# Optimization experiments

Hardware: AMD Instinct MI355X
Metric: run time of the kernel (lower is better)

## Reference

```python
import jax, jax.numpy as jnp
import numpy as np

DEPTH, DIM, DFF, VOCAB = 4, 512, 2048, 4096
EPS = 1e-5

def layernorm(x, w, b):
    mu = jnp.mean(x, axis=-1, keepdims=True)
    var = jnp.mean((x - mu) ** 2, axis=-1, keepdims=True)
    return (x - mu) * jax.lax.rsqrt(var + EPS) * w + b

def sconv(x, phazor_c, last_conv_c):
    # x: [B,L,dim] real; phazor_c, last_conv_c: [dim] complex
    B, L, D = x.shape
    r = jnp.abs(phazor_c)
    p = jnp.tanh(r) * jnp.exp(1j * jnp.angle(phazor_c))          # [dim]
    prog = p[None, :] ** jnp.arange(L, dtype=jnp.float32)[:, None]  # [L,dim]
    filt_fft = jnp.fft.fft(prog, n=2 * L, axis=0)                # [2L,dim]
    x_fft = jnp.fft.fft(x.astype(jnp.complex64), n=2 * L, axis=1)  # [B,2L,dim]
    conv = jnp.fft.ifft(filt_fft[None] * x_fft, axis=1)[:, :L]   # [B,L,dim]
    conv = conv + last_conv_c[None, None, :] * prog[None] * p[None, None, :]
    return conv.real.astype(x.dtype)

def setup_inputs() -> dict:
    key = jax.random.key(0)
    ks = jax.random.split(key, 20)
    f32 = jnp.float32
    inp = {}
    inp['x'] = jax.random.normal(ks[0], (2, 4096, VOCAB), dtype=f32)
    inp['Win'] = jax.random.normal(ks[1], (DIM, VOCAB), dtype=f32) * VOCAB ** -0.5
    inp['bin'] = jnp.zeros((DIM,), f32)
    inp['ln1_w'] = jnp.ones((DEPTH, DIM), f32)
    inp['ln1_b'] = jnp.zeros((DEPTH, DIM), f32)
    # phazor init: exp(2*pi*i*arange/dim)*|randn|
    ang = 2 * np.pi * jnp.arange(DIM, dtype=f32) / DIM
    mag = jnp.abs(jax.random.normal(ks[2], (DEPTH, DIM), dtype=f32))
    inp['phz_re'] = mag * jnp.cos(ang)[None]
    inp['phz_im'] = mag * jnp.sin(ang)[None]
    inp['lc_re'] = jax.random.normal(ks[3], (DEPTH, DIM), dtype=f32)
    inp['lc_im'] = jax.random.normal(ks[4], (DEPTH, DIM), dtype=f32)
    inp['sc_lin'] = jnp.ones((DEPTH, DIM), f32)
    inp['ln2_w'] = jnp.ones((DEPTH, DIM), f32)
    inp['ln2_b'] = jnp.zeros((DEPTH, DIM), f32)
    inp['W1'] = jax.random.normal(ks[5], (DEPTH, DFF, DIM), dtype=f32) * DIM ** -0.5
    inp['b1'] = jnp.zeros((DEPTH, DFF), f32)
    inp['W2'] = jax.random.normal(ks[6], (DEPTH, DIM, DFF), dtype=f32) * DFF ** -0.5
    inp['b2'] = jnp.zeros((DEPTH, DIM), f32)
    inp['lnl_w'] = jnp.ones((DIM,), f32)
    inp['lnl_b'] = jnp.zeros((DIM,), f32)
    inp['Wout'] = jax.random.normal(ks[7], (VOCAB, DIM), dtype=f32) * DIM ** -0.5
    inp['bout'] = jnp.zeros((VOCAB,), f32)
    return inp

def _forward(x, Win, bin, ln1_w, ln1_b, phz_re, phz_im, lc_re, lc_im, sc_lin,
             ln2_w, ln2_b, W1, b1, W2, b2, lnl_w, lnl_b, Wout, bout):
    h = jnp.einsum('blv,dv->bld', x, Win) + bin  # token_in

    def body(h, p):
        l1w, l1b, pr, pi, lr, li, scl, l2w, l2b, w1, b1_, w2, b2_ = p
        y = jax.nn.silu(layernorm(h, l1w, l1b))
        y = sconv(y, pr + 1j * pi, lr + 1j * li)
        h = h + y * scl
        y = layernorm(h, l2w, l2b)
        y = jax.nn.silu(jnp.einsum('bld,fd->blf', y, w1) + b1_)
        y = jnp.einsum('blf,df->bld', y, w2) + b2_
        return h + y, None

    xs = (ln1_w, ln1_b, phz_re, phz_im, lc_re, lc_im, sc_lin,
          ln2_w, ln2_b, W1, b1, W2, b2)
    h, _ = jax.lax.scan(body, h, xs)
    h = layernorm(h, lnl_w, lnl_b)
    return jnp.einsum('bld,vd->blv', h, Wout) + bout

def reference(x, Win, bin, ln1_w, ln1_b, phz_re, phz_im, lc_re, lc_im, sc_lin,
              ln2_w, ln2_b, W1, b1, W2, b2, lnl_w, lnl_b, Wout, bout):
    return _forward(x, Win, bin, ln1_w, ln1_b, phz_re, phz_im, lc_re, lc_im,
                    sc_lin, ln2_w, ln2_b, W1, b1, W2, b2, lnl_w, lnl_b, Wout, bout)
```

## Files before the change

### kernel.cpp

```cpp
#include <hip/hip_runtime.h>
#include <hip/hip_bf16.h>
#include <cstdint>
#include <cstddef>

#define DEPTH 4
#define DIM 512
#define DFF 2048
#define VOCAB 4096
#define NB 2
#define LSEQ 4096
#define MR (NB*LSEQ)
#define EPSL 1e-5f
#define NC 128
#define TCH 32

typedef __attribute__((ext_vector_type(8))) short  s8v;
typedef __attribute__((ext_vector_type(4))) float  f4v;
typedef __attribute__((ext_vector_type(8))) __bf16 bf8v;

__device__ __forceinline__ unsigned short f2b(float f) {
  union { float f; unsigned int u; } v; v.f = f;
  unsigned int r = v.u + 0x7FFFu + ((v.u >> 16) & 1u);
  return (unsigned short)(r >> 16);
}

__device__ __forceinline__ void gld16(const void* g, void* l) {
  __builtin_amdgcn_global_load_lds(
      (const __attribute__((address_space(1))) unsigned int*)(uintptr_t)g,
      (__attribute__((address_space(3))) unsigned int*)(uintptr_t)l,
      16, 0, 0);
}

__global__ void __launch_bounds__(256) cvt_f32_bf16(
    const float* __restrict__ in, unsigned short* __restrict__ out, int n8)
{
  int i = blockIdx.x * 256 + threadIdx.x;
  if (i >= n8) return;
  const f4v* p = (const f4v*)(in + (size_t)i * 8);
  f4v a = p[0], b = p[1];
  s8v o;
  o[0]=(short)f2b(a[0]); o[1]=(short)f2b(a[1]); o[2]=(short)f2b(a[2]); o[3]=(short)f2b(a[3]);
  o[4]=(short)f2b(b[0]); o[5]=(short)f2b(b[1]); o[6]=(short)f2b(b[2]); o[7]=(short)f2b(b[3]);
  *(s8v*)(out + (size_t)i * 8) = o;
}

template<int MODE>
__global__ void __launch_bounds__(256) ln_kernel(
    const float* __restrict__ x, const float* __restrict__ w, const float* __restrict__ b,
    float* __restrict__ outf, unsigned short* __restrict__ outb)
{
  int row  = blockIdx.x * 4 + (threadIdx.x >> 6);
  int lane = threadIdx.x & 63;
  const float* xp = x + (size_t)row * DIM + lane * 8;
  f4v v0 = *(const f4v*)xp;
  f4v v1 = *(const f4v*)(xp + 4);
  float s = 0.f, s2 = 0.f;
#pragma unroll
  for (int j = 0; j < 4; ++j) { s += v0[j]; s2 += v0[j]*v0[j]; s += v1[j]; s2 += v1[j]*v1[j]; }
#pragma unroll
  for (int off = 32; off; off >>= 1) { s += __shfl_xor(s, off, 64); s2 += __shfl_xor(s2, off, 64); }
  float mu = s * (1.f / DIM);
  float rs = rsqrtf(s2 * (1.f / DIM) - mu * mu + EPSL);
  int c = lane * 8;
  f4v w0 = *(const f4v*)(w + c), w1 = *(const f4v*)(w + c + 4);
  f4v b0 = *(const f4v*)(b + c), b1 = *(const f4v*)(b + c + 4);
  float ov[8];
#pragma unroll
  for (int j = 0; j < 8; ++j) {
    float xv = (j < 4) ? v0[j] : v1[j - 4];
    float wv = (j < 4) ? w0[j] : w1[j - 4];
    float bv = (j < 4) ? b0[j] : b1[j - 4];
    float o = (xv - mu) * rs * wv + bv;
    if (MODE == 0) o = o / (1.f + __expf(-o));
    ov[j] = o;
  }
  if (MODE == 0) {
    f4v o0 = {ov[0], ov[1], ov[2], ov[3]};
    f4v o1 = {ov[4], ov[5], ov[6], ov[7]};
    *(f4v*)(outf + (size_t)row * DIM + c)     = o0;
    *(f4v*)(outf + (size_t)row * DIM + c + 4) = o1;
  } else {
    s8v o;
#pragma unroll
    for (int j = 0; j < 8; ++j) o[j] = (short)f2b(ov[j]);
    *(s8v*)(outb + (size_t)row * DIM + c) = o;
  }
}

__device__ __forceinline__ void phz2p(float re, float im, float& pre, float& pim) {
  float r = sqrtf(re * re + im * im);
  float t = (r > 1e-20f) ? (tanhf(r) / r) : 1.0f;
  pre = t * re; pim = t * im;
}

__global__ void __launch_bounds__(256) scan_a(
    const float* __restrict__ y, const float* __restrict__ pr, const float* __restrict__ pi,
    float* __restrict__ stA)
{
  int d = blockIdx.z * 256 + threadIdx.x;
  int b = blockIdx.y, c = blockIdx.x;
  float pre, pim; phz2p(pr[d], pi[d], pre, pim);
  const float* yp = y + ((size_t)b * LSEQ + (size_t)c * TCH) * DIM + d;
  float sre = 0.f, sim = 0.f;
#pragma unroll 8
  for (int j = 0; j < TCH; ++j) {
    float xv = yp[(size_t)j * DIM];
    float nre = fmaf(pre, sre, fmaf(-pim, sim, xv));
    float nim = fmaf(pre, sim, pim * sre);
    sre = nre; sim = nim;
  }
  size_t o = (((size_t)b * NC + c) * DIM + d) * 2;
  stA[o] = sre; stA[o + 1] = sim;
}

__global__ void __launch_bounds__(256) scan_b(
    const float* __restrict__ stA, float* __restrict__ carry,
    const float* __restrict__ pr, const float* __restrict__ pi,
    const float* __restrict__ lcr, const float* __restrict__ lci)
{
  int idx = blockIdx.x * 256 + threadIdx.x;
  int b = idx >> 9, d = idx & (DIM - 1);
  float pre, pim; phz2p(pr[d], pi[d], pre, pim);
  float qre = pre, qim = pim;
#pragma unroll
  for (int t = 0; t < 5; ++t) { float nr = qre*qre - qim*qim; float ni = 2.f*qre*qim; qre = nr; qim = ni; }
  float cre = lcr[d], cim = lci[d];
#pragma unroll 4
  for (int c = 0; c < NC; ++c) {
    size_t o = (((size_t)b * NC + c) * DIM + d) * 2;
    carry[o] = cre; carry[o + 1] = cim;
    float are = stA[o], aim = stA[o + 1];
    float nr = fmaf(qre, cre, fmaf(-qim, cim, are));
    float ni = fmaf(qre, cim, fmaf(qim, cre, aim));
    cre = nr; cim = ni;
  }
}

__global__ void __launch_bounds__(256) scan_c(
    const float* __restrict__ y, float* __restrict__ h, const float* __restrict__ carry,
    const float* __restrict__ pr, const float* __restrict__ pi,
    const float* __restrict__ scl)
{
  int d = blockIdx.z * 256 + threadIdx.x;
  int b = blockIdx.y, c = blockIdx.x;
  float pre, pim; phz2p(pr[d], pi[d], pre, pim);
  size_t o = (((size_t)b * NC + c) * DIM + d) * 2;
  float sre = carry[o], sim = carry[o + 1];
  float sc = scl[d];
  const float* yp = y + ((size_t)b * LSEQ + (size_t)c * TCH) * DIM + d;
  float*       hp = h + ((size_t)b * LSEQ + (size_t)c * TCH) * DIM + d;
#pragma unroll 8
  for (int j = 0; j < TCH; ++j) {
    float xv = yp[(size_t)j * DIM];
    float nre = fmaf(pre, sre, fmaf(-pim, sim, xv));
    float nim = fmaf(pre, sim, pim * sre);
    sre = nre; sim = nim;
    hp[(size_t)j * DIM] += sre * sc;
  }
}

template<int EPI, int BN, int AF32>
__global__ void __launch_bounds__(256, BN == 64 ? 2 : 3) gemm_bt(
    const void* __restrict__ Ap, const unsigned short* __restrict__ Bm,
    const float* __restrict__ bias,
    float* __restrict__ Cf, unsigned short* __restrict__ Cb,
    int N, int K)
{
  constexpr int WN = BN / 2;
  constexpr int NJ = WN / 16;
  __shared__ unsigned short As[2][128 * 32];
  __shared__ unsigned short Bs[2][BN * 32];
  const int tid  = threadIdx.x;
  const int lane = tid & 63, wave = tid >> 6;
  const int wm = wave >> 1, wn = wave & 1;
  const int fr = lane & 15, fq = lane >> 4;

  int bx, by;
  {
    int gx = gridDim.x;
    int nwg = gx * gridDim.y;
    int b = blockIdx.y * gx + blockIdx.x;
    int lid = (b & 7) * (nwg >> 3) + (b >> 3);
    bx = lid % gx; by = lid / gx;
  }
  const int m0 = by * 128, n0 = bx * BN;

  f4v acc[4][NJ];
#pragma unroll
  for (int i = 0; i < 4; ++i)
#pragma unroll
    for (int j = 0; j < NJ; ++j) acc[i][j] = (f4v){0.f, 0.f, 0.f, 0.f};

  const int nkt = K >> 5;

  f4v areg[2][2];
  auto loadA = [&](int k0) {
    const float* Ab = (const float*)Ap + (size_t)m0 * K + k0;
#pragma unroll
    for (int r = 0; r < 2; ++r) {
      int idx = r * 256 + tid;
      int row = idx >> 2, col = (idx & 3) << 3;
      const float* p = Ab + (size_t)row * K + col;
      areg[r][0] = *(const f4v*)p;
      areg[r][1] = *(const f4v*)(p + 4);
    }
  };
  auto writeA = [&](int buf) {
#pragma unroll
    for (int r = 0; r < 2; ++r) {
      int idx = r * 256 + tid;
      s8v o;
#pragma unroll
      for (int j = 0; j < 4; ++j) {
        o[j]     = (short)f2b(areg[r][0][j]);
        o[4 + j] = (short)f2b(areg[r][1][j]);
      }
      *(s8v*)&As[buf][idx * 8] = o;
    }
  };
  auto stageA16 = [&](int buf, int k0) {
    const unsigned short* Ab = (const unsigned short*)Ap + (size_t)m0 * K + k0;
#pragma unroll
    for (int r = 0; r < 2; ++r) {
      int idx = r * 256 + tid;
      int row = idx >> 2, col = (idx & 3) << 3;
      gld16(Ab + (size_t)row * K + col, &As[buf][idx * 8]);
    }
  };
  auto stageB = [&](int buf, int k0) {
    const unsigned short* Bb = Bm + (size_t)n0 * K + k0;
#pragma unroll
    for (int r = 0; r < BN / 64; ++r) {
      int idx = r * 256 + tid;
      int row = idx >> 2, col = (idx & 3) << 3;
      gld16(Bb + (size_t)row * K + col, &Bs[buf][idx * 8]);
    }
  };

  if constexpr (AF32) loadA(0); else stageA16(0, 0);
  stageB(0, 0);
  if constexpr (AF32) writeA(0);
  __syncthreads();

  for (int kt = 0; kt < nkt; ++kt) {
    int cur = kt & 1;
    bool pf = (kt + 1 < nkt);
    if (pf) {
      if constexpr (AF32) loadA((kt + 1) << 5);
      else stageA16(cur ^ 1, (kt + 1) << 5);
      stageB(cur ^ 1, (kt + 1) << 5);
    }
    bf8v av[4], bv[NJ];
#pragma unroll
    for (int i = 0; i < 4; ++i)
      av[i] = *(const bf8v*)&As[cur][(wm * 64 + i * 16 + fr) * 32 + fq * 8];
#pragma unroll
    for (int j = 0; j < NJ; ++j)
      bv[j] = *(const bf8v*)&Bs[cur][(wn * WN + j * 16 + fr) * 32 + fq * 8];
#pragma unroll
    for (int i = 0; i < 4; ++i)
#pragma unroll
      for (int j = 0; j < NJ; ++j)
        acc[i][j] = __builtin_amdgcn_mfma_f32_16x16x32_bf16(av[i], bv[j], acc[i][j], 0, 0, 0);
    if (pf) { if constexpr (AF32) writeA(cur ^ 1); }
    __syncthreads();
  }

#pragma unroll
  for (int j = 0; j < NJ; ++j) {
    const int col = n0 + wn * WN + j * 16 + fr;
    const float bsv = bias[col];
#pragma unroll
    for (int i = 0; i < 4; ++i) {
#pragma unroll
      for (int r = 0; r < 4; ++r) {
        const int row = m0 + wm * 64 + i * 16 + fq * 4 + r;
        const size_t off = (size_t)row * N + col;
        float v = acc[i][j][r] + bsv;
        if constexpr (EPI == 0) {
          Cf[off] = v;
        } else if constexpr (EPI == 1) {
          float sv = v / (1.f + __expf(-v));
          Cb[off] = f2b(sv);
        } else {
          Cf[off] = Cf[off] + v;
        }
      }
    }
  }
}

extern "C" void kernel_launch(void* const* d_in, const int* in_sizes, int n_in,
                              void* d_out, int out_size, void* d_ws, size_t ws_size,
                              hipStream_t stream)
{
  (void)in_sizes; (void)n_in; (void)out_size; (void)ws_size;
  const float* x    = (const float*)d_in[0];
  const float* Win  = (const float*)d_in[1];
  const float* bin  = (const float*)d_in[2];
  const float* ln1w = (const float*)d_in[3];
  const float* ln1b = (const float*)d_in[4];
  const float* phzr = (const float*)d_in[5];
  const float* phzi = (const float*)d_in[6];
  const float* lcr  = (const float*)d_in[7];
  const float* lci  = (const float*)d_in[8];
  const float* scl  = (const float*)d_in[9];
  const float* ln2w = (const float*)d_in[10];
  const float* ln2b = (const float*)d_in[11];
  const float* W1   = (const float*)d_in[12];
  const float* b1   = (const float*)d_in[13];
  const float* W2   = (const float*)d_in[14];
  const float* b2   = (const float*)d_in[15];
  const float* lnlw = (const float*)d_in[16];
  const float* lnlb = (const float*)d_in[17];
  const float* Wout = (const float*)d_in[18];
  const float* bout = (const float*)d_in[19];

  char* wsp = (char*)d_ws;
  auto alloc = [&](size_t bytes) { char* p = wsp; wsp += (bytes + 255) & ~(size_t)255; return p; };
  float*          h     = (float*)alloc((size_t)MR * DIM * 4);
  float*          y     = (float*)alloc((size_t)MR * DIM * 4);
  unsigned short* yb    = (unsigned short*)alloc((size_t)MR * DIM * 2);
  unsigned short* Winb  = (unsigned short*)alloc((size_t)DIM * VOCAB * 2);
  unsigned short* W1b   = (unsigned short*)alloc((size_t)DEPTH * DFF * DIM * 2);
  unsigned short* W2b   = (unsigned short*)alloc((size_t)DEPTH * DIM * DFF * 2);
  unsigned short* Woutb = (unsigned short*)alloc((size_t)VOCAB * DIM * 2);
  float*          stA   = (float*)alloc((size_t)NB * NC * DIM * 2 * 4);
  float*          carry = (float*)alloc((size_t)NB * NC * DIM * 2 * 4);

  unsigned short* act1 = (unsigned short*)d_out;

  dim3 blk(256);
  cvt_f32_bf16<<<dim3((DIM * VOCAB) / 2048), blk, 0, stream>>>(Win, Winb, DIM * VOCAB / 8);
  cvt_f32_bf16<<<dim3((DEPTH * DFF * DIM) / 2048), blk, 0, stream>>>(W1, W1b, DEPTH * DFF * DIM / 8);
  cvt_f32_bf16<<<dim3((DEPTH * DFF * DIM) / 2048), blk, 0, stream>>>(W2, W2b, DEPTH * DIM * DFF / 8);
  cvt_f32_bf16<<<dim3((VOCAB * DIM) / 2048), blk, 0, stream>>>(Wout, Woutb, VOCAB * DIM / 8);

  gemm_bt<0, 64, 1><<<dim3(DIM / 64, MR / 128), blk, 0, stream>>>(
      x, Winb, bin, h, nullptr, DIM, VOCAB);

  for (int l = 0; l < DEPTH; ++l) {
    ln_kernel<0><<<dim3(MR / 4), blk, 0, stream>>>(h, ln1w + l * DIM, ln1b + l * DIM, y, nullptr);
    scan_a<<<dim3(NC, NB, DIM / 256), blk, 0, stream>>>(y, phzr + l * DIM, phzi + l * DIM, stA);
    scan_b<<<dim3((NB * DIM) / 256), blk, 0, stream>>>(stA, carry, phzr + l * DIM, phzi + l * DIM,
                                                       lcr + l * DIM, lci + l * DIM);
    scan_c<<<dim3(NC, NB, DIM / 256), blk, 0, stream>>>(y, h, carry, phzr + l * DIM, phzi + l * DIM,
                                                        scl + l * DIM);
    ln_kernel<1><<<dim3(MR / 4), blk, 0, stream>>>(h, ln2w + l * DIM, ln2b + l * DIM, nullptr, yb);
    gemm_bt<1, 128, 0><<<dim3(DFF / 128, MR / 128), blk, 0, stream>>>(
        yb, W1b + (size_t)l * DFF * DIM, b1 + l * DFF, nullptr, act1, DFF, DIM);
    gemm_bt<2, 64, 0><<<dim3(DIM / 64, MR / 128), blk, 0, stream>>>(
        act1, W2b + (size_t)l * DIM * DFF, b2 + l * DIM, h, nullptr, DIM, DFF);
  }
  ln_kernel<1><<<dim3(MR / 4), blk, 0, stream>>>(h, lnlw, lnlb, nullptr, yb);
  gemm_bt<0, 128, 0><<<dim3(VOCAB / 128, MR / 128), blk, 0, stream>>>(
      yb, Woutb, bout, (float*)d_out, nullptr, VOCAB, DIM);
}
```

Before: 649.9 us.

## Split-K the narrow N=512 GEMMs into four partials with a reduce kernel

The token-in GEMM (K=4096) and the W2 GEMM (K=2048) now use a 128x128 tile with split-K over four z-slices. Each slice writes fp32 partials into scratch space inside the output buffer, and a new reduce kernel sums them, adds the bias and optionally the residual. This is meant to fix low occupancy and parallelism, since the N=512 GEMMs previously launched only 8x64 blocks with a long K loop. The cost is extra partial-sum memory traffic (4x MR x 512 floats written and read back) and one additional launch per GEMM. Launch bounds are also raised to 4 waves per SIMD.

```diff
diff --git a/kernel.cpp b/kernel.cpp
--- a/kernel.cpp
+++ b/kernel.cpp
@@ -159,21 +159,20 @@
   }
 }
 
-template<int EPI, int BN, int AF32>
-__global__ void __launch_bounds__(256, BN == 64 ? 2 : 3) gemm_bt(
+template<int EPI, int AF32>
+__global__ void __launch_bounds__(256, 4) gemm_bt(
     const void* __restrict__ Ap, const unsigned short* __restrict__ Bm,
     const float* __restrict__ bias,
     float* __restrict__ Cf, unsigned short* __restrict__ Cb,
-    int N, int K)
-{
-  constexpr int WN = BN / 2;
-  constexpr int NJ = WN / 16;
+    int N, int Keff, int lda, int ldb)
+{
   __shared__ unsigned short As[2][128 * 32];
-  __shared__ unsigned short Bs[2][BN * 32];
+  __shared__ unsigned short Bs[2][128 * 32];
   const int tid  = threadIdx.x;
   const int lane = tid & 63, wave = tid >> 6;
   const int wm = wave >> 1, wn = wave & 1;
   const int fr = lane & 15, fq = lane >> 4;
+  const int bz = blockIdx.z;
 
   int bx, by;
   {
@@ -183,24 +182,25 @@
     int lid = (b & 7) * (nwg >> 3) + (b >> 3);
     bx = lid % gx; by = lid / gx;
   }
-  const int m0 = by * 128, n0 = bx * BN;
-
-  f4v acc[4][NJ];
+  const int m0 = by * 128, n0 = bx * 128;
+  const int koff = bz * Keff;
+
+  f4v acc[4][4];
 #pragma unroll
   for (int i = 0; i < 4; ++i)
 #pragma unroll
-    for (int j = 0; j < NJ; ++j) acc[i][j] = (f4v){0.f, 0.f, 0.f, 0.f};
-
-  const int nkt = K >> 5;
+    for (int j = 0; j < 4; ++j) acc[i][j] = (f4v){0.f, 0.f, 0.f, 0.f};
+
+  const int nkt = Keff >> 5;
 
   f4v areg[2][2];
   auto loadA = [&](int k0) {
-    const float* Ab = (const float*)Ap + (size_t)m0 * K + k0;
+    const float* Ab = (const float*)Ap + (size_t)m0 * lda + koff + k0;
 #pragma unroll
     for (int r = 0; r < 2; ++r) {
       int idx = r * 256 + tid;
       int row = idx >> 2, col = (idx & 3) << 3;
-      const float* p = Ab + (size_t)row * K + col;
+      const float* p = Ab + (size_t)row * lda + col;
       areg[r][0] = *(const f4v*)p;
       areg[r][1] = *(const f4v*)(p + 4);
     }
@@ -219,21 +219,21 @@
     }
   };
   auto stageA16 = [&](int buf, int k0) {
-    const unsigned short* Ab = (const unsigned short*)Ap + (size_t)m0 * K + k0;
+    const unsigned short* Ab = (const unsigned short*)Ap + (size_t)m0 * lda + koff + k0;
 #pragma unroll
     for (int r = 0; r < 2; ++r) {
       int idx = r * 256 + tid;
       int row = idx >> 2, col = (idx & 3) << 3;
-      gld16(Ab + (size_t)row * K + col, &As[buf][idx * 8]);
+      gld16(Ab + (size_t)row * lda + col, &As[buf][idx * 8]);
     }
   };
   auto stageB = [&](int buf, int k0) {
-    const unsigned short* Bb = Bm + (size_t)n0 * K + k0;
-#pragma unroll
-    for (int r = 0; r < BN / 64; ++r) {
+    const unsigned short* Bb = Bm + (size_t)n0 * ldb + koff + k0;
+#pragma unroll
+    for (int r = 0; r < 2; ++r) {
       int idx = r * 256 + tid;
       int row = idx >> 2, col = (idx & 3) << 3;
-      gld16(Bb + (size_t)row * K + col, &Bs[buf][idx * 8]);
+      gld16(Bb + (size_t)row * ldb + col, &Bs[buf][idx * 8]);
     }
   };
 
@@ -250,26 +250,27 @@
       else stageA16(cur ^ 1, (kt + 1) << 5);
       stageB(cur ^ 1, (kt + 1) << 5);
     }
-    bf8v av[4], bv[NJ];
+    bf8v av[4], bv[4];
 #pragma unroll
     for (int i = 0; i < 4; ++i)
       av[i] = *(const bf8v*)&As[cur][(wm * 64 + i * 16 + fr) * 32 + fq * 8];
 #pragma unroll
-    for (int j = 0; j < NJ; ++j)
-      bv[j] = *(const bf8v*)&Bs[cur][(wn * WN + j * 16 + fr) * 32 + fq * 8];
+    for (int j = 0; j < 4; ++j)
+      bv[j] = *(const bf8v*)&Bs[cur][(wn * 64 + j * 16 + fr) * 32 + fq * 8];
 #pragma unroll
     for (int i = 0; i < 4; ++i)
 #pragma unroll
-      for (int j = 0; j < NJ; ++j)
+      for (int j = 0; j < 4; ++j)
         acc[i][j] = __builtin_amdgcn_mfma_f32_16x16x32_bf16(av[i], bv[j], acc[i][j], 0, 0, 0);
     if (pf) { if constexpr (AF32) writeA(cur ^ 1); }
     __syncthreads();
   }
 
-#pragma unroll
-  for (int j = 0; j < NJ; ++j) {
-    const int col = n0 + wn * WN + j * 16 + fr;
-    const float bsv = bias[col];
+  const size_t pbase = (EPI == 3) ? (size_t)bz * MR * N : 0;
+#pragma unroll
+  for (int j = 0; j < 4; ++j) {
+    const int col = n0 + wn * 64 + j * 16 + fr;
+    const float bsv = (EPI == 3) ? 0.f : bias[col];
 #pragma unroll
     for (int i = 0; i < 4; ++i) {
 #pragma unroll
@@ -283,11 +284,28 @@
           float sv = v / (1.f + __expf(-v));
           Cb[off] = f2b(sv);
         } else {
-          Cf[off] = Cf[off] + v;
+          Cf[pbase + off] = v;
         }
       }
     }
   }
+}
+
+template<int RES>
+__global__ void __launch_bounds__(256) reduce_sk(
+    const float* __restrict__ parts, const float* __restrict__ bias,
+    float* __restrict__ out)
+{
+  size_t i = ((size_t)blockIdx.x * 256 + threadIdx.x) * 4;
+  const size_t st = (size_t)MR * DIM;
+  f4v v = *(const f4v*)(parts + i);
+  v += *(const f4v*)(parts + st + i);
+  v += *(const f4v*)(parts + 2 * st + i);
+  v += *(const f4v*)(parts + 3 * st + i);
+  int c = (int)(i & (DIM - 1));
+  v += *(const f4v*)(bias + c);
+  if (RES) v += *(const f4v*)(out + i);
+  *(f4v*)(out + i) = v;
 }
 
 extern "C" void kernel_launch(void* const* d_in, const int* in_sizes, int n_in,
@@ -328,7 +346,8 @@
   float*          stA   = (float*)alloc((size_t)NB * NC * DIM * 2 * 4);
   float*          carry = (float*)alloc((size_t)NB * NC * DIM * 2 * 4);
 
-  unsigned short* act1 = (unsigned short*)d_out;
+  unsigned short* act1  = (unsigned short*)d_out;
+  float*          parts = (float*)((char*)d_out + ((size_t)40 << 20));
 
   dim3 blk(256);
   cvt_f32_bf16<<<dim3((DIM * VOCAB) / 2048), blk, 0, stream>>>(Win, Winb, DIM * VOCAB / 8);
@@ -336,8 +355,9 @@
   cvt_f32_bf16<<<dim3((DEPTH * DFF * DIM) / 2048), blk, 0, stream>>>(W2, W2b, DEPTH * DIM * DFF / 8);
   cvt_f32_bf16<<<dim3((VOCAB * DIM) / 2048), blk, 0, stream>>>(Wout, Woutb, VOCAB * DIM / 8);
 
-  gemm_bt<0, 64, 1><<<dim3(DIM / 64, MR / 128), blk, 0, stream>>>(
-      x, Winb, bin, h, nullptr, DIM, VOCAB);
+  gemm_bt<3, 1><<<dim3(DIM / 128, MR / 128, 4), blk, 0, stream>>>(
+      x, Winb, nullptr, parts, nullptr, DIM, VOCAB / 4, VOCAB, VOCAB);
+  reduce_sk<0><<<dim3(MR * DIM / 1024), blk, 0, stream>>>(parts, bin, h);
 
   for (int l = 0; l < DEPTH; ++l) {
     ln_kernel<0><<<dim3(MR / 4), blk, 0, stream>>>(h, ln1w + l * DIM, ln1b + l * DIM, y, nullptr);
@@ -347,12 +367,13 @@
     scan_c<<<dim3(NC, NB, DIM / 256), blk, 0, stream>>>(y, h, carry, phzr + l * DIM, phzi + l * DIM,
                                                         scl + l * DIM);
     ln_kernel<1><<<dim3(MR / 4), blk, 0, stream>>>(h, ln2w + l * DIM, ln2b + l * DIM, nullptr, yb);
-    gemm_bt<1, 128, 0><<<dim3(DFF / 128, MR / 128), blk, 0, stream>>>(
-        yb, W1b + (size_t)l * DFF * DIM, b1 + l * DFF, nullptr, act1, DFF, DIM);
-    gemm_bt<2, 64, 0><<<dim3(DIM / 64, MR / 128), blk, 0, stream>>>(
-        act1, W2b + (size_t)l * DIM * DFF, b2 + l * DIM, h, nullptr, DIM, DFF);
+    gemm_bt<1, 0><<<dim3(DFF / 128, MR / 128, 1), blk, 0, stream>>>(
+        yb, W1b + (size_t)l * DFF * DIM, b1 + l * DFF, nullptr, act1, DFF, DIM, DIM, DIM);
+    gemm_bt<3, 0><<<dim3(DIM / 128, MR / 128, 4), blk, 0, stream>>>(
+        act1, W2b + (size_t)l * DIM * DFF, nullptr, parts, nullptr, DIM, DFF / 4, DFF, DFF);
+    reduce_sk<1><<<dim3(MR * DIM / 1024), blk, 0, stream>>>(parts, b2 + l * DIM, h);
   }
   ln_kernel<1><<<dim3(MR / 4), blk, 0, stream>>>(h, lnlw, lnlb, nullptr, yb);
-  gemm_bt<0, 128, 0><<<dim3(VOCAB / 128, MR / 128), blk, 0, stream>>>(
-      yb, Woutb, bout, (float*)d_out, nullptr, VOCAB, DIM);
-}
+  gemm_bt<0, 0><<<dim3(VOCAB / 128, MR / 128, 1), blk, 0, stream>>>(
+      yb, Woutb, bout, (float*)d_out, nullptr, VOCAB, DIM, DIM, DIM);
+}
```

Measured after the change: 668.5 us. 1.03x slower.
